# Kernel tuning notes

Hardware: AMD Instinct MI355X
Metric: run time of the kernel (lower is better)

The kernel has to match this reference:

```python
import jax, jax.numpy as jnp
import numpy as np

NUM_NODES = 10000
NUM_EDGES = 640000
IN_FEAT = 128
OUT_FEAT = 128


def setup_inputs() -> dict:
    key = jax.random.key(0)
    k_x, k_e, k_w = jax.random.split(key, 3)
    x = jax.random.normal(k_x, (NUM_NODES, IN_FEAT), dtype=jnp.float32)
    edge_index = jax.random.randint(k_e, (2, NUM_EDGES), 0, NUM_NODES, dtype=jnp.int64)
    # Xavier-uniform W, zeros B (as in the torch init)
    limit = float(np.sqrt(6.0 / (IN_FEAT + OUT_FEAT)))
    W = jax.random.uniform(k_w, (OUT_FEAT, IN_FEAT), dtype=jnp.float32, minval=-limit, maxval=limit)
    B = jnp.zeros((OUT_FEAT, IN_FEAT), dtype=jnp.float32)
    return {"x": x, "edge_index": edge_index, "W": W, "B": B}


def reference(x, edge_index, W, B):
    num_nodes = x.shape[0]
    src, dst = edge_index[0], edge_index[1]
    # gather messages from source nodes, scatter-add into destination nodes
    messages = x[src]  # [num_edges, in_feat]
    agg = jax.ops.segment_sum(messages, dst, num_segments=num_nodes)  # [num_nodes, in_feat]
    # in-degree normalization (zero-degree nodes -> divide by 1)
    deg = jax.ops.segment_sum(jnp.ones_like(dst, dtype=x.dtype), dst, num_segments=num_nodes)
    deg = jnp.where(deg == 0, jnp.asarray(1.0, x.dtype), deg)
    agg = agg / deg[:, None]
    # dual linear combine: messages @ W.T + x @ B.T
    return agg @ W.T + x @ B.T
```

## Files before the change

### kernel.cpp

```cpp
#include <hip/hip_runtime.h>

#define NUM_NODES 10000
#define NUM_EDGES 640000
#define FEAT 128
#define K2 256
#define NPB 32
#define NBUCK 313
#define NBIN 157
#define EPB 4096
#define SCAP 40
#define DEG_MAX 128
#define ASTRIDE 136

using bf16x8 = __attribute__((ext_vector_type(8))) short;
using f32x4 = __attribute__((ext_vector_type(4))) float;

static __device__ inline unsigned short f2bf(float f) {
  union { float f; unsigned int u; } v;
  v.f = f;
  unsigned int r = v.u + 0x7FFF + ((v.u >> 16) & 1);
  return (unsigned short)(r >> 16);
}
static __device__ inline float bf2f(unsigned short u) {
  union { unsigned int u; float f; } v;
  v.u = ((unsigned int)u) << 16;
  return v.f;
}

__global__ __launch_bounds__(256) void convert_bin_kernel(
    const float* __restrict__ x,
    const float* __restrict__ W,
    const float* __restrict__ B,
    const int* __restrict__ src,
    const int* __restrict__ dst,
    unsigned short* __restrict__ Xbf,
    unsigned short* __restrict__ Bbuf,
    unsigned int* __restrict__ staging,
    int* __restrict__ cntmat) {
  __shared__ int hist[NBUCK];
  int blk = blockIdx.x;
  int tid = threadIdx.x;
  if (blk < NBIN) {
    int ebase = blk * EPB;
    for (int t = tid; t < NBUCK; t += 256) hist[t] = 0;
    __syncthreads();
    int s[16], d[16];
#pragma unroll
    for (int i = 0; i < 16; ++i) {
      int e = ebase + tid + i * 256;
      if (e < NUM_EDGES) {
        s[i] = src[e];
        d[i] = dst[e];
      } else {
        s[i] = -1;
        d[i] = 0;
      }
    }
    __syncthreads();
#pragma unroll
    for (int i = 0; i < 16; ++i) {
      if (s[i] >= 0) {
        int bkt = d[i] >> 5;
        int r = atomicAdd(&hist[bkt], 1);
        if (r < SCAP)
          staging[((size_t)bkt * NBIN + blk) * SCAP + r] =
              ((unsigned int)(d[i] & 31) << 16) | (unsigned int)s[i];
      }
    }
    __syncthreads();
    for (int t = tid; t < NBUCK; t += 256)
      cntmat[(size_t)blk * NBUCK + t] = hist[t];
  } else if (blk < 157 + 1250) {
    int base = ((blk - NBIN) * 256 + tid) * 4;
    float4 v = *(const float4*)(x + base);
    ushort4 o;
    o.x = f2bf(v.x); o.y = f2bf(v.y); o.z = f2bf(v.z); o.w = f2bf(v.w);
    *(ushort4*)(Xbf + base) = o;
  } else {
    int base = ((blk - 1407) * 256 + tid) * 4;
    const float* srcp;
    size_t dstoff;
    if (base < FEAT * FEAT) {
      int o = base >> 7, k = base & 127;
      srcp = W + base;
      dstoff = (size_t)o * K2 + k;
    } else {
      int b = base - FEAT * FEAT;
      int o = b >> 7, k = b & 127;
      srcp = B + b;
      dstoff = (size_t)o * K2 + FEAT + k;
    }
    float4 v = *(const float4*)srcp;
    ushort4 ov;
    ov.x = f2bf(v.x); ov.y = f2bf(v.y); ov.z = f2bf(v.z); ov.w = f2bf(v.w);
    *(ushort4*)(Bbuf + dstoff) = ov;
  }
}

__global__ __launch_bounds__(1024) void agg_gemm_kernel(
    const unsigned int* __restrict__ staging,
    const int* __restrict__ cntmat,
    const unsigned short* __restrict__ Xbf,
    const unsigned short* __restrict__ Bbuf,
    float* __restrict__ out) {
  __shared__ unsigned short lcsr[NPB * DEG_MAX];
  __shared__ int lcnt[NPB];
  __shared__ int scnt[NBIN];
  __shared__ __attribute__((aligned(16))) unsigned short aggA[NPB * ASTRIDE];
  int b = blockIdx.x;
  int tid = threadIdx.x;
  if (tid < NPB) lcnt[tid] = 0;
  for (int t = tid; t < NBIN; t += 1024) {
    int c = cntmat[(size_t)t * NBUCK + b];
    scnt[t] = (c > SCAP) ? SCAP : c;
  }
  __syncthreads();
  const unsigned int* stb = staging + (size_t)b * (NBIN * SCAP);
  for (int i = tid; i < NBIN * SCAP; i += 1024) {
    int blk = i / SCAP;
    int slot = i - blk * SCAP;
    if (slot < scnt[blk]) {
      unsigned int e = stb[i];
      int dl = e >> 16;
      int pos = atomicAdd(&lcnt[dl], 1);
      if (pos < DEG_MAX)
        lcsr[dl * DEG_MAX + pos] = (unsigned short)(e & 0xFFFF);
    }
  }
  __syncthreads();

  int grp = tid >> 5;
  int lane = tid & 31;
  {
    int deg = (b * NPB + grp < NUM_NODES) ? lcnt[grp] : 0;
    if (deg > DEG_MAX) deg = DEG_MAX;
    const unsigned short* row = lcsr + grp * DEG_MAX;
    float a0[4] = {0.f, 0.f, 0.f, 0.f};
    float a1[4] = {0.f, 0.f, 0.f, 0.f};
    float a2[4] = {0.f, 0.f, 0.f, 0.f};
    float a3[4] = {0.f, 0.f, 0.f, 0.f};
    int e = 0;
    for (; e + 4 <= deg; e += 4) {
      int s0 = row[e], s1 = row[e + 1], s2 = row[e + 2], s3 = row[e + 3];
      ushort4 v0 = *(const ushort4*)(Xbf + (size_t)s0 * FEAT + lane * 4);
      ushort4 v1 = *(const ushort4*)(Xbf + (size_t)s1 * FEAT + lane * 4);
      ushort4 v2 = *(const ushort4*)(Xbf + (size_t)s2 * FEAT + lane * 4);
      ushort4 v3 = *(const ushort4*)(Xbf + (size_t)s3 * FEAT + lane * 4);
      a0[0] += bf2f(v0.x); a0[1] += bf2f(v0.y); a0[2] += bf2f(v0.z); a0[3] += bf2f(v0.w);
      a1[0] += bf2f(v1.x); a1[1] += bf2f(v1.y); a1[2] += bf2f(v1.z); a1[3] += bf2f(v1.w);
      a2[0] += bf2f(v2.x); a2[1] += bf2f(v2.y); a2[2] += bf2f(v2.z); a2[3] += bf2f(v2.w);
      a3[0] += bf2f(v3.x); a3[1] += bf2f(v3.y); a3[2] += bf2f(v3.z); a3[3] += bf2f(v3.w);
    }
    for (; e < deg; ++e) {
      int s0 = row[e];
      ushort4 v0 = *(const ushort4*)(Xbf + (size_t)s0 * FEAT + lane * 4);
      a0[0] += bf2f(v0.x); a0[1] += bf2f(v0.y); a0[2] += bf2f(v0.z); a0[3] += bf2f(v0.w);
    }
    float sc = (deg == 0) ? 1.0f : (1.0f / (float)deg);
    ushort4 o;
    o.x = f2bf((a0[0] + a1[0] + a2[0] + a3[0]) * sc);
    o.y = f2bf((a0[1] + a1[1] + a2[1] + a3[1]) * sc);
    o.z = f2bf((a0[2] + a1[2] + a2[2] + a3[2]) * sc);
    o.w = f2bf((a0[3] + a1[3] + a2[3] + a3[3]) * sc);
    *(ushort4*)(aggA + grp * ASTRIDE + lane * 4) = o;
  }
  __syncthreads();

  int w = tid >> 6;
  int l = tid & 63;
  int r = l & 15;
  int g = l >> 4;
  int rt = w >> 3;
  int ct = w & 7;
  int arl = rt * 16 + r;
  int arg = b * NPB + arl;
  if (arg >= NUM_NODES) arg = NUM_NODES - 1;

  f32x4 acc = {};
#pragma unroll
  for (int ks = 0; ks < 8; ++ks) {
    bf16x8 a;
    if (ks < 4)
      a = *(const bf16x8*)(aggA + arl * ASTRIDE + ks * 32 + g * 8);
    else
      a = *(const bf16x8*)(Xbf + (size_t)arg * FEAT + (ks - 4) * 32 + g * 8);
    int kb = ks * 32 + g * 8;
    bf16x8 bb = *(const bf16x8*)(Bbuf + (size_t)(ct * 16 + r) * K2 + kb);
    acc = __builtin_amdgcn_mfma_f32_16x16x32_bf16(a, bb, acc, 0, 0, 0);
  }

#pragma unroll
  for (int j = 0; j < 4; ++j) {
    int rr = b * NPB + rt * 16 + g * 4 + j;
    if (rr < NUM_NODES) out[(size_t)rr * FEAT + ct * 16 + r] = acc[j];
  }
}

extern "C" void kernel_launch(void* const* d_in, const int* in_sizes, int n_in,
                              void* d_out, int out_size, void* d_ws, size_t ws_size,
                              hipStream_t stream) {
  const float* x = (const float*)d_in[0];
  const int* ei = (const int*)d_in[1];
  const float* W = (const float*)d_in[2];
  const float* B = (const float*)d_in[3];
  float* out = (float*)d_out;

  unsigned short* Xbf = (unsigned short*)d_ws;
  unsigned short* Bbuf = Xbf + (size_t)NUM_NODES * FEAT;
  unsigned int* staging = (unsigned int*)(Bbuf + (size_t)FEAT * K2);
  int* cntmat = (int*)(staging + (size_t)NBUCK * NBIN * SCAP);

  const int* src = ei;
  const int* dst = ei + NUM_EDGES;

  convert_bin_kernel<<<1439, 256, 0, stream>>>(x, W, B, src, dst, Xbf, Bbuf,
                                               staging, cntmat);
  agg_gemm_kernel<<<NBUCK, 1024, 0, stream>>>(staging, cntmat, Xbf, Bbuf, out);
}
```

Baseline: 104.8 us.

## Stage edge bins in LDS with coalesced flush; widen gather to 16-byte loads

The binning kernel now writes bucketed edges into a shared-memory staging array and flushes it to global memory with coalesced uint4 stores. Previously each edge was scattered to global memory on its own. The staging layout becomes bin-major, so the aggregation kernel reads each bucket's slots with a strided index. The gather phase now gives each node 32 lanes: 16 lanes load 8 bf16 features each (16-byte loads), two parity halves split the edges, and a shuffle combines the halves. The cost is about 50KB of LDS per binning block, which lowers occupancy, plus less contiguous reads in the aggregation kernel.

After: 102.9 us. About the same (-1.8%).

```diff
diff --git a/kernel.cpp b/kernel.cpp
--- a/kernel.cpp
+++ b/kernel.cpp
@@ -15,6 +15,8 @@
 using bf16x8 = __attribute__((ext_vector_type(8))) short;
 using f32x4 = __attribute__((ext_vector_type(4))) float;
 
+typedef struct { unsigned short s[8]; } ushort8_t;
+
 static __device__ inline unsigned short f2bf(float f) {
   union { float f; unsigned int u; } v;
   v.f = f;
@@ -38,46 +40,40 @@
     unsigned int* __restrict__ staging,
     int* __restrict__ cntmat) {
   __shared__ int hist[NBUCK];
+  __shared__ __attribute__((aligned(16))) unsigned int lstage[NBUCK * SCAP];
   int blk = blockIdx.x;
   int tid = threadIdx.x;
   if (blk < NBIN) {
     int ebase = blk * EPB;
     for (int t = tid; t < NBUCK; t += 256) hist[t] = 0;
     __syncthreads();
-    int s[16], d[16];
 #pragma unroll
     for (int i = 0; i < 16; ++i) {
       int e = ebase + tid + i * 256;
       if (e < NUM_EDGES) {
-        s[i] = src[e];
-        d[i] = dst[e];
-      } else {
-        s[i] = -1;
-        d[i] = 0;
-      }
-    }
-    __syncthreads();
-#pragma unroll
-    for (int i = 0; i < 16; ++i) {
-      if (s[i] >= 0) {
-        int bkt = d[i] >> 5;
+        int s = src[e];
+        int d = dst[e];
+        int bkt = d >> 5;
         int r = atomicAdd(&hist[bkt], 1);
         if (r < SCAP)
-          staging[((size_t)bkt * NBIN + blk) * SCAP + r] =
-              ((unsigned int)(d[i] & 31) << 16) | (unsigned int)s[i];
+          lstage[bkt * SCAP + r] =
+              ((unsigned int)(d & 31) << 16) | (unsigned int)s;
       }
     }
     __syncthreads();
+    uint4* gs = (uint4*)(staging + (size_t)blk * (NBUCK * SCAP));
+    const uint4* ls = (const uint4*)lstage;
+    for (int i = tid; i < NBUCK * SCAP / 4; i += 256) gs[i] = ls[i];
     for (int t = tid; t < NBUCK; t += 256)
       cntmat[(size_t)blk * NBUCK + t] = hist[t];
-  } else if (blk < 157 + 1250) {
+  } else if (blk < NBIN + 1250) {
     int base = ((blk - NBIN) * 256 + tid) * 4;
     float4 v = *(const float4*)(x + base);
     ushort4 o;
     o.x = f2bf(v.x); o.y = f2bf(v.y); o.z = f2bf(v.z); o.w = f2bf(v.w);
     *(ushort4*)(Xbf + base) = o;
   } else {
-    int base = ((blk - 1407) * 256 + tid) * 4;
+    int base = ((blk - NBIN - 1250) * 256 + tid) * 4;
     const float* srcp;
     size_t dstoff;
     if (base < FEAT * FEAT) {
@@ -115,12 +111,11 @@
     scnt[t] = (c > SCAP) ? SCAP : c;
   }
   __syncthreads();
-  const unsigned int* stb = staging + (size_t)b * (NBIN * SCAP);
   for (int i = tid; i < NBIN * SCAP; i += 1024) {
     int blk = i / SCAP;
     int slot = i - blk * SCAP;
     if (slot < scnt[blk]) {
-      unsigned int e = stb[i];
+      unsigned int e = staging[((size_t)blk * NBUCK + b) * SCAP + slot];
       int dl = e >> 16;
       int pos = atomicAdd(&lcnt[dl], 1);
       if (pos < DEG_MAX)
@@ -129,40 +124,46 @@
   }
   __syncthreads();
 
-  int grp = tid >> 5;
-  int lane = tid & 31;
   {
-    int deg = (b * NPB + grp < NUM_NODES) ? lcnt[grp] : 0;
+    int w = tid >> 6;
+    int wl = tid & 63;
+    int sgp = wl >> 4;
+    int sl = wl & 15;
+    int nl = w * 2 + (sgp >> 1);
+    int par = sgp & 1;
+    int deg = lcnt[nl];
     if (deg > DEG_MAX) deg = DEG_MAX;
-    const unsigned short* row = lcsr + grp * DEG_MAX;
-    float a0[4] = {0.f, 0.f, 0.f, 0.f};
-    float a1[4] = {0.f, 0.f, 0.f, 0.f};
-    float a2[4] = {0.f, 0.f, 0.f, 0.f};
-    float a3[4] = {0.f, 0.f, 0.f, 0.f};
-    int e = 0;
-    for (; e + 4 <= deg; e += 4) {
-      int s0 = row[e], s1 = row[e + 1], s2 = row[e + 2], s3 = row[e + 3];
-      ushort4 v0 = *(const ushort4*)(Xbf + (size_t)s0 * FEAT + lane * 4);
-      ushort4 v1 = *(const ushort4*)(Xbf + (size_t)s1 * FEAT + lane * 4);
-      ushort4 v2 = *(const ushort4*)(Xbf + (size_t)s2 * FEAT + lane * 4);
-      ushort4 v3 = *(const ushort4*)(Xbf + (size_t)s3 * FEAT + lane * 4);
-      a0[0] += bf2f(v0.x); a0[1] += bf2f(v0.y); a0[2] += bf2f(v0.z); a0[3] += bf2f(v0.w);
-      a1[0] += bf2f(v1.x); a1[1] += bf2f(v1.y); a1[2] += bf2f(v1.z); a1[3] += bf2f(v1.w);
-      a2[0] += bf2f(v2.x); a2[1] += bf2f(v2.y); a2[2] += bf2f(v2.z); a2[3] += bf2f(v2.w);
-      a3[0] += bf2f(v3.x); a3[1] += bf2f(v3.y); a3[2] += bf2f(v3.z); a3[3] += bf2f(v3.w);
-    }
-    for (; e < deg; ++e) {
+    const unsigned short* row = lcsr + nl * DEG_MAX;
+    const size_t foff = (size_t)sl * 8;
+    float a0[8] = {0.f, 0.f, 0.f, 0.f, 0.f, 0.f, 0.f, 0.f};
+    float a1[8] = {0.f, 0.f, 0.f, 0.f, 0.f, 0.f, 0.f, 0.f};
+    int e = par;
+    for (; e + 2 < deg; e += 4) {
       int s0 = row[e];
-      ushort4 v0 = *(const ushort4*)(Xbf + (size_t)s0 * FEAT + lane * 4);
-      a0[0] += bf2f(v0.x); a0[1] += bf2f(v0.y); a0[2] += bf2f(v0.z); a0[3] += bf2f(v0.w);
+      int s1 = row[e + 2];
+      ushort8_t v0 = *(const ushort8_t*)(Xbf + (size_t)s0 * FEAT + foff);
+      ushort8_t v1 = *(const ushort8_t*)(Xbf + (size_t)s1 * FEAT + foff);
+#pragma unroll
+      for (int k = 0; k < 8; ++k) a0[k] += bf2f(v0.s[k]);
+#pragma unroll
+      for (int k = 0; k < 8; ++k) a1[k] += bf2f(v1.s[k]);
+    }
+    if (e < deg) {
+      int s0 = row[e];
+      ushort8_t v0 = *(const ushort8_t*)(Xbf + (size_t)s0 * FEAT + foff);
+#pragma unroll
+      for (int k = 0; k < 8; ++k) a0[k] += bf2f(v0.s[k]);
     }
     float sc = (deg == 0) ? 1.0f : (1.0f / (float)deg);
-    ushort4 o;
-    o.x = f2bf((a0[0] + a1[0] + a2[0] + a3[0]) * sc);
-    o.y = f2bf((a0[1] + a1[1] + a2[1] + a3[1]) * sc);
-    o.z = f2bf((a0[2] + a1[2] + a2[2] + a3[2]) * sc);
-    o.w = f2bf((a0[3] + a1[3] + a2[3] + a3[3]) * sc);
-    *(ushort4*)(aggA + grp * ASTRIDE + lane * 4) = o;
+    ushort8_t o;
+#pragma unroll
+    for (int k = 0; k < 8; ++k) {
+      float v = a0[k] + a1[k];
+      v += __shfl_xor(v, 16, 64);
+      o.s[k] = f2bf(v * sc);
+    }
+    if (par == 0)
+      *(ushort8_t*)(aggA + nl * ASTRIDE + sl * 8) = o;
   }
   __syncthreads();
 
@@ -208,7 +209,7 @@
   unsigned short* Xbf = (unsigned short*)d_ws;
   unsigned short* Bbuf = Xbf + (size_t)NUM_NODES * FEAT;
   unsigned int* staging = (unsigned int*)(Bbuf + (size_t)FEAT * K2);
-  int* cntmat = (int*)(staging + (size_t)NBUCK * NBIN * SCAP);
+  int* cntmat = (int*)(staging + (size_t)NBIN * NBUCK * SCAP);
 
   const int* src = ei;
   const int* dst = ei + NUM_EDGES;
```
